# Performance work log

Hardware: AMD Instinct MI355X
Metric: run time of the kernel (lower is better)

The kernel has to match this reference:

```python
import jax, jax.numpy as jnp
import numpy as np

COST_CLASS, COST_MASK, COST_DICE = 2.0, 5.0, 5.0
NUM_POINTS = 12544

def setup_inputs() -> dict:
    key = jax.random.key(0)
    k1, k2, k3, k4, k5 = jax.random.split(key, 5)
    bs, Q, K = 4, 100, 134
    H = W = 256
    M = 80
    P = H * W
    pred_logits = jax.random.normal(k1, (bs, Q, K), dtype=jnp.float32)
    pred_masks = jax.random.normal(k2, (bs, Q, H, W), dtype=jnp.float32)
    tgt_labels = jax.random.randint(k3, (M,), 0, K - 1, dtype=jnp.int32)
    # binary target masks, stored as float (matches .float() in torch code)
    tgt_masks = (jax.random.uniform(k4, (M, H, W)) > 0.5).astype(jnp.float32)
    # random subset of points without replacement (torch.randperm[:num_points])
    point_idx = jax.random.permutation(k5, P)[:NUM_POINTS].astype(jnp.int32)
    return {"pred_logits": pred_logits, "pred_masks": pred_masks,
            "tgt_labels": tgt_labels, "tgt_masks": tgt_masks,
            "point_idx": point_idx}

def reference(pred_logits, pred_masks, tgt_labels, tgt_masks, point_idx):
    bs, Q, K = pred_logits.shape
    N = bs * Q
    M = tgt_masks.shape[0]
    Pn = point_idx.shape[0]

    # class cost: -p[n, tgt_id[m]]
    out_prob = jax.nn.softmax(pred_logits.reshape(N, K), axis=-1)
    tgt_ids = jnp.clip(tgt_labels.astype(jnp.int32), 0, K - 1)
    cost_class = -out_prob[:, tgt_ids]                      # (N, M)

    # sampled mask logits / targets
    x = pred_masks.reshape(N, -1)[:, point_idx]             # (N, Pn) logits
    y = tgt_masks.reshape(M, -1)[:, point_idx]              # (M, Pn) binary float

    # BCE-with-logits cost, separable form:
    # mean_p[softplus(x) - x*y] = mean_p softplus(x) - (x @ y^T)/Pn
    sp_mean = jnp.mean(jax.nn.softplus(x), axis=-1)         # (N,)
    xy = jnp.einsum('np,mp->nm', x, y)                      # (N, M)
    cost_mask = sp_mean[:, None] - xy / Pn

    # dice cost
    s = jax.nn.sigmoid(x)                                   # (N, Pn)
    numer = 2.0 * jnp.einsum('np,mp->nm', s, y)             # (N, M)
    denom = jnp.sum(s, axis=-1)[:, None] + jnp.sum(y, axis=-1)[None, :]
    cost_dice = 1.0 - (numer + 1.0) / (denom + 1.0)

    C = COST_CLASS * cost_class + COST_MASK * cost_mask + COST_DICE * cost_dice
    return C.reshape(bs, Q, M)
```

## Files before the change

kernel.cpp:

```cpp
#include <hip/hip_runtime.h>
#include <math.h>

#define N_ROWS 400
#define M_ROWS 80
#define K_CLS  134
#define PN     12544
#define PFULL  65536
#define NSUB   25
#define TSTEPS 392
#define KSPLIT 56
#define TPB    7

typedef __attribute__((ext_vector_type(4))) float  f32x4;
typedef __attribute__((ext_vector_type(8))) __bf16 bf16x8;

__device__ __forceinline__ float wave_reduce_sum(float v) {
#pragma unroll
    for (int off = 32; off > 0; off >>= 1) v += __shfl_down(v, off, 64);
    return v;
}

__global__ void softmax_stats_kernel(const float* __restrict__ logits,
                                     float* __restrict__ rowmax,
                                     float* __restrict__ rowsum) {
    int n = blockIdx.x;
    const float* row = logits + n * K_CLS;
    int l = threadIdx.x;
    float mx = -1e30f;
    for (int k = l; k < K_CLS; k += 64) mx = fmaxf(mx, row[k]);
#pragma unroll
    for (int off = 32; off > 0; off >>= 1) mx = fmaxf(mx, __shfl_down(mx, off, 64));
    mx = __shfl(mx, 0, 64);
    float se = 0.f;
    for (int k = l; k < K_CLS; k += 64) se += expf(row[k] - mx);
    se = wave_reduce_sum(se);
    if (l == 0) { rowmax[n] = mx; rowsum[n] = se; }
}

__global__ __launch_bounds__(512) void gather_x_kernel(
        const float* __restrict__ pred_masks, const int* __restrict__ point_idx,
        __bf16* __restrict__ Xb, __bf16* __restrict__ Sb,
        float* __restrict__ spsum, float* __restrict__ ssum) {
    int n = blockIdx.x;
    const float* row = pred_masks + (size_t)n * PFULL;
    __bf16* xrow = Xb + (size_t)n * PN;
    __bf16* srow = Sb + (size_t)n * PN;
    float ssp = 0.f, sss = 0.f;
#pragma unroll 4
    for (int p = threadIdx.x; p < PN; p += 512) {
        int idx = point_idx[p];
        float x  = row[idx];
        float ax = fabsf(x);
        float e  = __expf(-ax);
        float inv = __builtin_amdgcn_rcpf(1.0f + e);
        float sig = (x >= 0.f) ? inv : e * inv;
        float sp  = fmaxf(x, 0.f) + __logf(1.0f + e);
        xrow[p] = (__bf16)x;
        srow[p] = (__bf16)sig;
        ssp += sp; sss += sig;
    }
    __shared__ float sm1[8], sm2[8];
    float w1 = wave_reduce_sum(ssp), w2 = wave_reduce_sum(sss);
    int lane = threadIdx.x & 63, wid = threadIdx.x >> 6;
    if (lane == 0) { sm1[wid] = w1; sm2[wid] = w2; }
    __syncthreads();
    if (threadIdx.x == 0) {
        float a = 0.f, b = 0.f;
#pragma unroll
        for (int i = 0; i < 8; ++i) { a += sm1[i]; b += sm2[i]; }
        spsum[n] = a; ssum[n] = b;
    }
}

__global__ __launch_bounds__(256) void gather_y_kernel(
        const float* __restrict__ tgt_masks, const int* __restrict__ point_idx,
        __bf16* __restrict__ Yb, float* __restrict__ ysum) {
    int j = blockIdx.x / 49;
    int tchunk = blockIdx.x % 49;
    int wave = threadIdx.x >> 6, lane = threadIdx.x & 63;
    int colL = lane & 15, quad = lane >> 4;
    int m = 16 * j + colL;
    const float* yrow = tgt_masks + (size_t)m * PFULL;
    bf16x8* out = (bf16x8*)Yb;
    float acc = 0.f;
#pragma unroll
    for (int u = 0; u < 2; ++u) {
        int t = tchunk * 8 + wave * 2 + u;
        int k0 = t * 32 + quad * 8;
        int idx[8];
        *(int4*)(idx)     = *(const int4*)(point_idx + k0);
        *(int4*)(idx + 4) = *(const int4*)(point_idx + k0 + 4);
        bf16x8 v;
#pragma unroll
        for (int jj = 0; jj < 8; ++jj) {
            float y = yrow[idx[jj]];
            v[jj] = (__bf16)y;
            acc += y;
        }
        out[(size_t)(t * 5 + j) * 64 + lane] = v;
    }
    acc += __shfl_down(acc, 32, 64);
    acc += __shfl_down(acc, 16, 64);
    if (quad == 0) atomicAdd(&ysum[m], acc);
}

__global__ __launch_bounds__(256) void mfma_gemm_kernel(
        const __bf16* __restrict__ Xb, const __bf16* __restrict__ Sb,
        const __bf16* __restrict__ Yb,
        float* __restrict__ xyacc, float* __restrict__ syacc) {
    int wave = threadIdx.x >> 6, lane = threadIdx.x & 63;
    int nsub = blockIdx.x * 4 + wave;
    int nclamp = nsub < NSUB ? nsub : NSUB - 1;
    int n0 = nclamp * 16;
    int colL = lane & 15, quad = lane >> 4;
    int tbase = blockIdx.y * TPB;

    const __bf16* xrow = Xb + (size_t)(n0 + colL) * PN;
    const __bf16* srow = Sb + (size_t)(n0 + colL) * PN;
    const bf16x8* Yfrag = (const bf16x8*)Yb;

    f32x4 accX[5], accS[5];
    f32x4 zero = {0.f, 0.f, 0.f, 0.f};
#pragma unroll
    for (int j = 0; j < 5; ++j) { accX[j] = zero; accS[j] = zero; }

    bf16x8 Abuf[2], Sbuf[2], Bbuf[2][5];
    auto load = [&](int i, int b) {
        int t = tbase + i;
        size_t ko = (size_t)t * 32 + quad * 8;
        Abuf[b] = *(const bf16x8*)(xrow + ko);
        Sbuf[b] = *(const bf16x8*)(srow + ko);
        const bf16x8* q = Yfrag + (size_t)(t * 5) * 64 + lane;
#pragma unroll
        for (int j = 0; j < 5; ++j) Bbuf[b][j] = q[(size_t)j * 64];
    };

    load(0, 0);
#pragma unroll
    for (int i = 0; i < TPB; ++i) {
        int b = i & 1;
        if (i + 1 < TPB) load(i + 1, b ^ 1);
#pragma unroll
        for (int j = 0; j < 5; ++j) {
            accX[j] = __builtin_amdgcn_mfma_f32_16x16x32_bf16(Abuf[b], Bbuf[b][j], accX[j], 0, 0, 0);
            accS[j] = __builtin_amdgcn_mfma_f32_16x16x32_bf16(Sbuf[b], Bbuf[b][j], accS[j], 0, 0, 0);
        }
    }

    if (nsub < NSUB) {
#pragma unroll
        for (int j = 0; j < 5; ++j)
#pragma unroll
            for (int r = 0; r < 4; ++r) {
                int n = n0 + quad * 4 + r;
                int m = 16 * j + colL;
                atomicAdd(&xyacc[n * M_ROWS + m], accX[j][r]);
                atomicAdd(&syacc[n * M_ROWS + m], accS[j][r]);
            }
    }
}

__global__ void combine_kernel(const float* __restrict__ logits,
                               const int* __restrict__ tgt_labels,
                               const float* __restrict__ rowmax,
                               const float* __restrict__ rowsum,
                               const float* __restrict__ spsum,
                               const float* __restrict__ ssum,
                               const float* __restrict__ ysum,
                               const float* __restrict__ xyacc,
                               const float* __restrict__ syacc,
                               float* __restrict__ out) {
    int idx = blockIdx.x * blockDim.x + threadIdx.x;
    if (idx >= N_ROWS * M_ROWS) return;
    int n = idx / M_ROWS, m = idx % M_ROWS;
    int tid = tgt_labels[m];
    tid = min(max(tid, 0), K_CLS - 1);
    float p = expf(logits[n * K_CLS + tid] - rowmax[n]) / rowsum[n];
    float cost_class = -p;
    float cost_mask = (spsum[n] - xyacc[idx]) * (1.0f / PN);
    float cost_dice = 1.f - (2.f * syacc[idx] + 1.f) / (ssum[n] + ysum[m] + 1.f);
    out[idx] = 2.f * cost_class + 5.f * cost_mask + 5.f * cost_dice;
}

extern "C" void kernel_launch(void* const* d_in, const int* in_sizes, int n_in,
                              void* d_out, int out_size, void* d_ws, size_t ws_size,
                              hipStream_t stream) {
    const float* pred_logits = (const float*)d_in[0];
    const float* pred_masks  = (const float*)d_in[1];
    const int*   tgt_labels  = (const int*)d_in[2];
    const float* tgt_masks   = (const float*)d_in[3];
    const int*   point_idx   = (const int*)d_in[4];
    float* out = (float*)d_out;

    char* ws = (char*)d_ws;
    size_t off = 0;
    auto carve = [&](size_t nbytes) {
        char* p = ws + off;
        off += (nbytes + 255) & ~(size_t)255;
        return p;
    };
    float* xyacc = (float*)carve((size_t)N_ROWS * M_ROWS * 4);
    float* syacc = (float*)carve((size_t)N_ROWS * M_ROWS * 4);
    float* ysum  = (float*)carve(M_ROWS * 4);
    size_t zero_bytes = off;
    float* spsum  = (float*)carve(N_ROWS * 4);
    float* ssum   = (float*)carve(N_ROWS * 4);
    float* rowmax = (float*)carve(N_ROWS * 4);
    float* rowsum = (float*)carve(N_ROWS * 4);
    __bf16* Xb = (__bf16*)carve((size_t)N_ROWS * PN * 2);
    __bf16* Sb = (__bf16*)carve((size_t)N_ROWS * PN * 2);
    __bf16* Yb = (__bf16*)carve((size_t)TSTEPS * 5 * 1024);
    (void)ws_size;

    hipMemsetAsync(xyacc, 0, zero_bytes, stream);
    gather_x_kernel<<<N_ROWS, 512, 0, stream>>>(pred_masks, point_idx, Xb, Sb, spsum, ssum);
    gather_y_kernel<<<5 * 49, 256, 0, stream>>>(tgt_masks, point_idx, Yb, ysum);
    softmax_stats_kernel<<<N_ROWS, 64, 0, stream>>>(pred_logits, rowmax, rowsum);
    dim3 grid((NSUB + 3) / 4, KSPLIT);
    mfma_gemm_kernel<<<grid, 256, 0, stream>>>(Xb, Sb, Yb, xyacc, syacc);
    combine_kernel<<<(N_ROWS * M_ROWS + 255) / 256, 256, 0, stream>>>(
        pred_logits, tgt_labels, rowmax, rowsum, spsum, ssum, ysum, xyacc, syacc, out);
}
```

Measured before the change: 252.2 us.

## Sort sampled point indices and fuse gather/softmax stages into one launch

Adds a single-block kernel that builds a flag bitmap of sampled points and emits them in ascending order, so the later gathers read pred_masks and tgt_masks with better locality. The sum over points is order-independent and the same permutation is applied to X and Y, so the results stay the same. It also fuses the X gather, Y gather and softmax stats into one launch, reduces ysum atomics through shared memory, and folds the zeroing memset into the sort kernel. The cost is an extra serial single-block kernel on the critical path.

```diff
diff --git a/kernel.cpp b/kernel.cpp
--- a/kernel.cpp
+++ b/kernel.cpp
@@ -11,8 +11,13 @@
 #define KSPLIT 56
 #define TPB    7
 
+#define GX_BLOCKS 400
+#define GY_BLOCKS 245
+#define SM_BLOCKS 50
+
 typedef __attribute__((ext_vector_type(4))) float  f32x4;
 typedef __attribute__((ext_vector_type(8))) __bf16 bf16x8;
+typedef __attribute__((ext_vector_type(4))) __bf16 bf16x4;
 
 __device__ __forceinline__ float wave_reduce_sum(float v) {
 #pragma unroll
@@ -20,88 +25,144 @@
     return v;
 }
 
-__global__ void softmax_stats_kernel(const float* __restrict__ logits,
-                                     float* __restrict__ rowmax,
-                                     float* __restrict__ rowsum) {
-    int n = blockIdx.x;
-    const float* row = logits + n * K_CLS;
-    int l = threadIdx.x;
-    float mx = -1e30f;
-    for (int k = l; k < K_CLS; k += 64) mx = fmaxf(mx, row[k]);
-#pragma unroll
-    for (int off = 32; off > 0; off >>= 1) mx = fmaxf(mx, __shfl_down(mx, off, 64));
-    mx = __shfl(mx, 0, 64);
-    float se = 0.f;
-    for (int k = l; k < K_CLS; k += 64) se += expf(row[k] - mx);
-    se = wave_reduce_sum(se);
-    if (l == 0) { rowmax[n] = mx; rowsum[n] = se; }
-}
-
-__global__ __launch_bounds__(512) void gather_x_kernel(
-        const float* __restrict__ pred_masks, const int* __restrict__ point_idx,
-        __bf16* __restrict__ Xb, __bf16* __restrict__ Sb,
-        float* __restrict__ spsum, float* __restrict__ ssum) {
-    int n = blockIdx.x;
-    const float* row = pred_masks + (size_t)n * PFULL;
-    __bf16* xrow = Xb + (size_t)n * PN;
-    __bf16* srow = Sb + (size_t)n * PN;
-    float ssp = 0.f, sss = 0.f;
-#pragma unroll 4
-    for (int p = threadIdx.x; p < PN; p += 512) {
-        int idx = point_idx[p];
-        float x  = row[idx];
-        float ax = fabsf(x);
-        float e  = __expf(-ax);
-        float inv = __builtin_amdgcn_rcpf(1.0f + e);
-        float sig = (x >= 0.f) ? inv : e * inv;
-        float sp  = fmaxf(x, 0.f) + __logf(1.0f + e);
-        xrow[p] = (__bf16)x;
-        srow[p] = (__bf16)sig;
-        ssp += sp; sss += sig;
-    }
-    __shared__ float sm1[8], sm2[8];
-    float w1 = wave_reduce_sum(ssp), w2 = wave_reduce_sum(sss);
-    int lane = threadIdx.x & 63, wid = threadIdx.x >> 6;
-    if (lane == 0) { sm1[wid] = w1; sm2[wid] = w2; }
-    __syncthreads();
-    if (threadIdx.x == 0) {
-        float a = 0.f, b = 0.f;
-#pragma unroll
-        for (int i = 0; i < 8; ++i) { a += sm1[i]; b += sm2[i]; }
-        spsum[n] = a; ssum[n] = b;
-    }
-}
-
-__global__ __launch_bounds__(256) void gather_y_kernel(
-        const float* __restrict__ tgt_masks, const int* __restrict__ point_idx,
-        __bf16* __restrict__ Yb, float* __restrict__ ysum) {
-    int j = blockIdx.x / 49;
-    int tchunk = blockIdx.x % 49;
-    int wave = threadIdx.x >> 6, lane = threadIdx.x & 63;
-    int colL = lane & 15, quad = lane >> 4;
-    int m = 16 * j + colL;
-    const float* yrow = tgt_masks + (size_t)m * PFULL;
-    bf16x8* out = (bf16x8*)Yb;
-    float acc = 0.f;
-#pragma unroll
-    for (int u = 0; u < 2; ++u) {
-        int t = tchunk * 8 + wave * 2 + u;
+__global__ __launch_bounds__(1024) void sel_sort_kernel(
+        const int* __restrict__ point_idx, int* __restrict__ sel,
+        float* __restrict__ zero_region, int zero_n) {
+    __shared__ unsigned int flagw[PFULL / 4];
+    __shared__ int wtot[16], wbase[16];
+    int tid = threadIdx.x;
+    for (int i = tid; i < PFULL / 4; i += 1024) flagw[i] = 0u;
+    for (int i = tid; i < zero_n; i += 1024) zero_region[i] = 0.f;
+    __syncthreads();
+    unsigned char* flag = (unsigned char*)flagw;
+    for (int i = tid; i < PN; i += 1024) flag[point_idx[i]] = 1;
+    __syncthreads();
+    unsigned int w[16];
+    int cnt = 0;
+#pragma unroll
+    for (int j = 0; j < 16; ++j) {
+        w[j] = flagw[tid * 16 + j];
+        cnt += (int)((w[j] * 0x01010101u) >> 24);
+    }
+    int lane = tid & 63, wid = tid >> 6;
+    int v = cnt;
+#pragma unroll
+    for (int off = 1; off < 64; off <<= 1) {
+        int u = __shfl_up(v, off, 64);
+        if (lane >= off) v += u;
+    }
+    if (lane == 63) wtot[wid] = v;
+    __syncthreads();
+    if (tid == 0) {
+        int run = 0;
+#pragma unroll
+        for (int i = 0; i < 16; ++i) { wbase[i] = run; run += wtot[i]; }
+    }
+    __syncthreads();
+    int base = wbase[wid] + (v - cnt);
+#pragma unroll
+    for (int j = 0; j < 16; ++j) {
+        unsigned int u = w[j];
+        int p0 = tid * 64 + j * 4;
+        if (u & 0x01u)       sel[base++] = p0;
+        if (u & 0x0100u)     sel[base++] = p0 + 1;
+        if (u & 0x010000u)   sel[base++] = p0 + 2;
+        if (u & 0x01000000u) sel[base++] = p0 + 3;
+    }
+}
+
+__global__ __launch_bounds__(512) void stage1_kernel(
+        const float* __restrict__ pred_masks, const float* __restrict__ tgt_masks,
+        const float* __restrict__ pred_logits, const int* __restrict__ sel,
+        __bf16* __restrict__ Xb, __bf16* __restrict__ Sb, __bf16* __restrict__ Yb,
+        float* __restrict__ spsum, float* __restrict__ ssum, float* __restrict__ ysum,
+        float* __restrict__ rowmax, float* __restrict__ rowsum) {
+    __shared__ float smem[128];
+    int b = blockIdx.x;
+    if (b < GX_BLOCKS) {
+        int n = b;
+        const float* row = pred_masks + (size_t)n * PFULL;
+        __bf16* xr = Xb + (size_t)n * PN;
+        __bf16* sr = Sb + (size_t)n * PN;
+        float ssp = 0.f, sss = 0.f;
+#pragma unroll
+        for (int it = 0; it < 7; ++it) {
+            int k0 = it * 2048 + (int)threadIdx.x * 4;
+            if (k0 < PN) {
+                int4 id = *(const int4*)(sel + k0);
+                float xs0 = row[id.x], xs1 = row[id.y], xs2 = row[id.z], xs3 = row[id.w];
+                float xs[4] = {xs0, xs1, xs2, xs3};
+                bf16x4 vx, vs;
+#pragma unroll
+                for (int q = 0; q < 4; ++q) {
+                    float x  = xs[q];
+                    float ax = fabsf(x);
+                    float e  = __expf(-ax);
+                    float inv = __builtin_amdgcn_rcpf(1.f + e);
+                    float sig = (x >= 0.f) ? inv : e * inv;
+                    float sp  = fmaxf(x, 0.f) + __logf(1.f + e);
+                    vx[q] = (__bf16)x; vs[q] = (__bf16)sig;
+                    ssp += sp; sss += sig;
+                }
+                *(bf16x4*)(xr + k0) = vx;
+                *(bf16x4*)(sr + k0) = vs;
+            }
+        }
+        float w1 = wave_reduce_sum(ssp), w2 = wave_reduce_sum(sss);
+        int lane = threadIdx.x & 63, wid = threadIdx.x >> 6;
+        if (lane == 0) { smem[wid] = w1; smem[8 + wid] = w2; }
+        __syncthreads();
+        if (threadIdx.x == 0) {
+            float a = 0.f, c = 0.f;
+#pragma unroll
+            for (int i = 0; i < 8; ++i) { a += smem[i]; c += smem[8 + i]; }
+            spsum[n] = a; ssum[n] = c;
+        }
+    } else if (b < GX_BLOCKS + GY_BLOCKS) {
+        int bb = b - GX_BLOCKS;
+        int j = bb / 49, tch = bb % 49;
+        int wave = threadIdx.x >> 6, lane = threadIdx.x & 63;
+        int colL = lane & 15, quad = lane >> 4;
+        int m = 16 * j + colL;
+        int t = tch * 8 + wave;
         int k0 = t * 32 + quad * 8;
+        const float* yrow = tgt_masks + (size_t)m * PFULL;
         int idx[8];
-        *(int4*)(idx)     = *(const int4*)(point_idx + k0);
-        *(int4*)(idx + 4) = *(const int4*)(point_idx + k0 + 4);
-        bf16x8 v;
+        *(int4*)(idx)     = *(const int4*)(sel + k0);
+        *(int4*)(idx + 4) = *(const int4*)(sel + k0 + 4);
+        bf16x8 v; float acc = 0.f;
 #pragma unroll
         for (int jj = 0; jj < 8; ++jj) {
             float y = yrow[idx[jj]];
             v[jj] = (__bf16)y;
             acc += y;
         }
-        out[(size_t)(t * 5 + j) * 64 + lane] = v;
-    }
-    acc += __shfl_down(acc, 32, 64);
-    acc += __shfl_down(acc, 16, 64);
-    if (quad == 0) atomicAdd(&ysum[m], acc);
+        ((bf16x8*)Yb)[(size_t)(t * 5 + j) * 64 + lane] = v;
+        acc += __shfl_down(acc, 32, 64);
+        acc += __shfl_down(acc, 16, 64);
+        if (quad == 0) smem[wave * 16 + colL] = acc;
+        __syncthreads();
+        if (threadIdx.x < 16) {
+            float s = 0.f;
+#pragma unroll
+            for (int wv = 0; wv < 8; ++wv) s += smem[wv * 16 + threadIdx.x];
+            atomicAdd(&ysum[16 * j + threadIdx.x], s);
+        }
+    } else {
+        int bb = b - GX_BLOCKS - GY_BLOCKS;
+        int wave = threadIdx.x >> 6, lane = threadIdx.x & 63;
+        int n = bb * 8 + wave;
+        const float* row = pred_logits + n * K_CLS;
+        float mx = -1e30f;
+        for (int k = lane; k < K_CLS; k += 64) mx = fmaxf(mx, row[k]);
+#pragma unroll
+        for (int off = 32; off > 0; off >>= 1) mx = fmaxf(mx, __shfl_down(mx, off, 64));
+        mx = __shfl(mx, 0, 64);
+        float se = 0.f;
+        for (int k = lane; k < K_CLS; k += 64) se += expf(row[k] - mx);
+        se = wave_reduce_sum(se);
+        if (lane == 0) { rowmax[n] = mx; rowsum[n] = se; }
+    }
 }
 
 __global__ __launch_bounds__(256) void mfma_gemm_kernel(
@@ -125,25 +186,25 @@
     for (int j = 0; j < 5; ++j) { accX[j] = zero; accS[j] = zero; }
 
     bf16x8 Abuf[2], Sbuf[2], Bbuf[2][5];
-    auto load = [&](int i, int b) {
+    auto load = [&](int i, int bb) {
         int t = tbase + i;
         size_t ko = (size_t)t * 32 + quad * 8;
-        Abuf[b] = *(const bf16x8*)(xrow + ko);
-        Sbuf[b] = *(const bf16x8*)(srow + ko);
+        Abuf[bb] = *(const bf16x8*)(xrow + ko);
+        Sbuf[bb] = *(const bf16x8*)(srow + ko);
         const bf16x8* q = Yfrag + (size_t)(t * 5) * 64 + lane;
 #pragma unroll
-        for (int j = 0; j < 5; ++j) Bbuf[b][j] = q[(size_t)j * 64];
+        for (int j = 0; j < 5; ++j) Bbuf[bb][j] = q[(size_t)j * 64];
     };
 
     load(0, 0);
 #pragma unroll
     for (int i = 0; i < TPB; ++i) {
-        int b = i & 1;
-        if (i + 1 < TPB) load(i + 1, b ^ 1);
+        int bb = i & 1;
+        if (i + 1 < TPB) load(i + 1, bb ^ 1);
 #pragma unroll
         for (int j = 0; j < 5; ++j) {
-            accX[j] = __builtin_amdgcn_mfma_f32_16x16x32_bf16(Abuf[b], Bbuf[b][j], accX[j], 0, 0, 0);
-            accS[j] = __builtin_amdgcn_mfma_f32_16x16x32_bf16(Sbuf[b], Bbuf[b][j], accS[j], 0, 0, 0);
+            accX[j] = __builtin_amdgcn_mfma_f32_16x16x32_bf16(Abuf[bb], Bbuf[bb][j], accX[j], 0, 0, 0);
+            accS[j] = __builtin_amdgcn_mfma_f32_16x16x32_bf16(Sbuf[bb], Bbuf[bb][j], accS[j], 0, 0, 0);
         }
     }
 
@@ -202,7 +263,8 @@
     float* xyacc = (float*)carve((size_t)N_ROWS * M_ROWS * 4);
     float* syacc = (float*)carve((size_t)N_ROWS * M_ROWS * 4);
     float* ysum  = (float*)carve(M_ROWS * 4);
-    size_t zero_bytes = off;
+    int zero_n = (int)(off / 4);
+    int*   sel    = (int*)carve(PN * 4);
     float* spsum  = (float*)carve(N_ROWS * 4);
     float* ssum   = (float*)carve(N_ROWS * 4);
     float* rowmax = (float*)carve(N_ROWS * 4);
@@ -210,12 +272,12 @@
     __bf16* Xb = (__bf16*)carve((size_t)N_ROWS * PN * 2);
     __bf16* Sb = (__bf16*)carve((size_t)N_ROWS * PN * 2);
     __bf16* Yb = (__bf16*)carve((size_t)TSTEPS * 5 * 1024);
-    (void)ws_size;
-
-    hipMemsetAsync(xyacc, 0, zero_bytes, stream);
-    gather_x_kernel<<<N_ROWS, 512, 0, stream>>>(pred_masks, point_idx, Xb, Sb, spsum, ssum);
-    gather_y_kernel<<<5 * 49, 256, 0, stream>>>(tgt_masks, point_idx, Yb, ysum);
-    softmax_stats_kernel<<<N_ROWS, 64, 0, stream>>>(pred_logits, rowmax, rowsum);
+    (void)ws_size; (void)in_sizes; (void)n_in; (void)out_size;
+
+    sel_sort_kernel<<<1, 1024, 0, stream>>>(point_idx, sel, xyacc, zero_n);
+    stage1_kernel<<<GX_BLOCKS + GY_BLOCKS + SM_BLOCKS, 512, 0, stream>>>(
+        pred_masks, tgt_masks, pred_logits, sel, Xb, Sb, Yb,
+        spsum, ssum, ysum, rowmax, rowsum);
     dim3 grid((NSUB + 3) / 4, KSPLIT);
     mfma_gemm_kernel<<<grid, 256, 0, stream>>>(Xb, Sb, Yb, xyacc, syacc);
     combine_kernel<<<(N_ROWS * M_ROWS + 255) / 256, 256, 0, stream>>>(
```

Result: faster. 222.6 us (-11.8%).
